# Performance work log

Measured on AMD Instinct MI355X. Metric: run time of the kernel, lower is better.

The kernel has to match this reference:

```python
import jax, jax.numpy as jnp
import numpy as np

B, D, F, K, S = 256, 1024, 4096, 8, 8  # batch, d_model, d_ffn, basis_count, cluster_size


def setup_inputs() -> dict:
    key = jax.random.key(0)
    ks = jax.random.split(key, 7)
    return {
        "x": jax.random.normal(ks[0], (B, D, 1, 1), dtype=jnp.float32),
        "gate_w": jax.random.normal(ks[1], (K, F, D), dtype=jnp.float32) * (D ** -0.5),
        "up_w": jax.random.normal(ks[2], (K, F, D), dtype=jnp.float32) * (D ** -0.5),
        "down_w": jax.random.normal(ks[3], (K, D, F), dtype=jnp.float32) * (F ** -0.5),
        "gate_coeff": jax.random.normal(ks[4], (S, K), dtype=jnp.float32) * (K ** -0.5),
        "up_coeff": jax.random.normal(ks[5], (S, K), dtype=jnp.float32) * (K ** -0.5),
        "down_coeff": jax.random.normal(ks[6], (S, K), dtype=jnp.float32) * (K ** -0.5),
    }


def reference(x, gate_w, up_w, down_w, gate_coeff, up_coeff, down_coeff):
    # x: [B, D, 1, 1] -> token vectors [B, D]  (1x1 convs == matmuls; conv biases are zero)
    b = x.shape[0]
    xs = x[:, :, 0, 0]
    # basis banks: [B, K, F]
    gate_bank = jnp.einsum('bd,kfd->bkf', xs, gate_w)
    up_bank = jnp.einsum('bd,kfd->bkf', xs, up_w)
    # per-slot coefficient contraction over basis dim K -> [B, S, F]
    gate = jnp.einsum('bkf,sk->bsf', gate_bank, gate_coeff)
    up = jnp.einsum('bkf,sk->bsf', up_bank, up_coeff)
    hidden = jax.nn.silu(gate) * up  # [B, S, F]
    # down basis bank: [B, S, K, D]
    down_bank = jnp.einsum('bsf,kdf->bskd', hidden, down_w)
    out = jnp.einsum('bskd,sk->bsd', down_bank, down_coeff)  # [B, S, D]
    # torch.cat over slots along channel dim -> [B, S*D, 1, 1]
    return out.reshape(b, -1, 1, 1)
```

## Files before the change

### kernel.cpp

```cpp
#include <hip/hip_runtime.h>

#define B_SZ 256
#define D_SZ 1024
#define F_SZ 4096
#define K_SZ 8
#define S_SZ 8
#define NW   (2 * K_SZ * F_SZ)
#define SD   (S_SZ * D_SZ)

typedef __attribute__((ext_vector_type(4))) float f32x4v;
typedef __attribute__((ext_vector_type(8))) short s16x8v;

#define SWZ(row, col) ((col) ^ (((row) & 7) << 3))

#define BAR() do {                                            \
    asm volatile("s_waitcnt lgkmcnt(0)" ::: "memory");        \
    __builtin_amdgcn_sched_barrier(0);                        \
    __builtin_amdgcn_s_barrier();                             \
    __builtin_amdgcn_sched_barrier(0);                        \
} while (0)

static __device__ __forceinline__ unsigned short f2bf(float f) {
    union { float f; unsigned u; } v; v.f = f;
    unsigned u = v.u;
    unsigned r = u + 0x7FFFu + ((u >> 16) & 1u);
    return (unsigned short)(r >> 16);
}
static __device__ __forceinline__ float bf2f(unsigned short h) {
    union { unsigned u; float f; } v; v.u = ((unsigned)h) << 16;
    return v.f;
}

__global__ __launch_bounds__(256) void k_cvt_x(const float* __restrict__ x,
                                               unsigned short* __restrict__ xs) {
    int g = blockIdx.x * 256 + threadIdx.x;
    float4 v = reinterpret_cast<const float4*>(x)[g];
    ushort4 h;
    h.x = f2bf(v.x); h.y = f2bf(v.y); h.z = f2bf(v.z); h.w = f2bf(v.w);
    reinterpret_cast<ushort4*>(xs)[g] = h;
}

__global__ __launch_bounds__(512)
void k_bank_gemm(const unsigned short* __restrict__ xs,
                 const float* __restrict__ gw,
                 const float* __restrict__ uw,
                 unsigned short* __restrict__ bank) {
    __shared__ unsigned short As[2][256 * 64];
    __shared__ unsigned short Bs[2][128 * 64];

    const int tid  = threadIdx.x;
    const int lane = tid & 63;
    const int wid  = tid >> 6;
    const int wm   = wid >> 1;
    const int wn   = wid & 1;
    const int n0   = blockIdx.x * 128;

    const int ar = tid >> 3;
    const int ac = (tid * 8) & 63;
    const int br = tid >> 4;
    const int bc = (tid * 4) & 63;

    f32x4v acc[4][4];
    #pragma unroll
    for (int i = 0; i < 4; i++)
        #pragma unroll
        for (int j = 0; j < 4; j++) {
            f32x4v z = {0.f, 0.f, 0.f, 0.f};
            acc[i][j] = z;
        }

    uint4  a0[4], a1[4];
    float4 b0[4], b1[4];

#define K1_LOAD_A(dst, kt) do { _Pragma("unroll")                              \
    for (int i = 0; i < 4; i++)                                                \
        dst[i] = *reinterpret_cast<const uint4*>(                              \
            xs + (size_t)(ar + i * 64) * D_SZ + (kt) * 64 + ac); } while (0)

#define K1_LOAD_B(dst, kt) do { _Pragma("unroll")                              \
    for (int i = 0; i < 4; i++) {                                              \
        int n = n0 + br + i * 32;                                              \
        const float* src = (n < K_SZ * F_SZ)                                   \
            ? (gw + (size_t)n * D_SZ)                                          \
            : (uw + (size_t)(n - K_SZ * F_SZ) * D_SZ);                         \
        dst[i] = *reinterpret_cast<const float4*>(src + (kt) * 64 + bc);       \
    } } while (0)

#define K1_WRITE_A(buf, src) do { _Pragma("unroll")                            \
    for (int i = 0; i < 4; i++) {                                              \
        int r = ar + i * 64;                                                   \
        *reinterpret_cast<uint4*>(&As[buf][(r << 6) + SWZ(r, ac)]) = src[i];   \
    } } while (0)

#define K1_WRITE_B(buf, src) do { _Pragma("unroll")                            \
    for (int i = 0; i < 4; i++) {                                              \
        int r = br + i * 32; ushort4 h;                                        \
        h.x = f2bf(src[i].x); h.y = f2bf(src[i].y);                            \
        h.z = f2bf(src[i].z); h.w = f2bf(src[i].w);                            \
        *reinterpret_cast<ushort4*>(&Bs[buf][(r << 6) + SWZ(r, bc)]) = h;      \
    } } while (0)

#define K1_COMPUTE(buf) do { _Pragma("unroll")                                 \
    for (int kk = 0; kk < 2; kk++) {                                           \
        const int kof = kk * 32 + (lane >> 4) * 8;                             \
        s16x8v af[4], bfv[4];                                                  \
        _Pragma("unroll") for (int i = 0; i < 4; i++) {                        \
            int row = wm * 64 + i * 16 + (lane & 15);                          \
            af[i] = *reinterpret_cast<const s16x8v*>(                          \
                &As[buf][(row << 6) + SWZ(row, kof)]); }                       \
        _Pragma("unroll") for (int j = 0; j < 4; j++) {                        \
            int col = wn * 64 + j * 16 + (lane & 15);                          \
            bfv[j] = *reinterpret_cast<const s16x8v*>(                         \
                &Bs[buf][(col << 6) + SWZ(col, kof)]); }                       \
        _Pragma("unroll") for (int i = 0; i < 4; i++)                          \
            _Pragma("unroll") for (int j = 0; j < 4; j++)                      \
                acc[i][j] = __builtin_amdgcn_mfma_f32_16x16x32_bf16(           \
                    af[i], bfv[j], acc[i][j], 0, 0, 0);                        \
    } } while (0)

    K1_LOAD_A(a0, 0); K1_LOAD_B(b0, 0);
    K1_LOAD_A(a1, 1); K1_LOAD_B(b1, 1);
    K1_WRITE_A(0, a0); K1_WRITE_B(0, b0);
    BAR();

    #pragma unroll 1
    for (int kt2 = 0; kt2 < 8; kt2++) {
        const int kt = kt2 * 2;
        if (kt + 2 < 16) { K1_LOAD_A(a0, kt + 2); K1_LOAD_B(b0, kt + 2); }
        K1_COMPUTE(0);
        K1_WRITE_A(1, a1); K1_WRITE_B(1, b1);
        BAR();
        if (kt + 3 < 16) { K1_LOAD_A(a1, kt + 3); K1_LOAD_B(b1, kt + 3); }
        K1_COMPUTE(1);
        if (kt + 2 < 16) {
            K1_WRITE_A(0, a0); K1_WRITE_B(0, b0);
            BAR();
        }
    }

    const int r0 = (lane >> 4) * 4;
    const int c0 = lane & 15;
    #pragma unroll
    for (int i = 0; i < 4; i++) {
        int rowb = wm * 64 + i * 16 + r0;
        #pragma unroll
        for (int j = 0; j < 4; j++) {
            int col = n0 + wn * 64 + j * 16 + c0;
            #pragma unroll
            for (int r = 0; r < 4; r++)
                bank[(size_t)(rowb + r) * NW + col] = f2bf(acc[i][j][r]);
        }
    }
#undef K1_LOAD_A
#undef K1_LOAD_B
#undef K1_WRITE_A
#undef K1_WRITE_B
#undef K1_COMPUTE
}

__global__ __launch_bounds__(256)
void k_combine_silu(const unsigned short* __restrict__ bank,
                    const float* __restrict__ gcoef,
                    const float* __restrict__ ucoef,
                    unsigned short* __restrict__ hid) {
    __shared__ float sg[64], su[64];
    int tid = threadIdx.x;
    if (tid < 64) { sg[tid] = gcoef[tid]; su[tid] = ucoef[tid]; }
    __syncthreads();

    int g  = blockIdx.x * 256 + tid;
    int fq = g & (F_SZ / 4 - 1);
    int b  = g >> 10;
    size_t base = (size_t)b * NW + fq * 4;

    float gv[8][4], uv[8][4];
    #pragma unroll
    for (int k = 0; k < 8; k++) {
        ushort4 tg = *reinterpret_cast<const ushort4*>(bank + base + (size_t)k * F_SZ);
        ushort4 tu = *reinterpret_cast<const ushort4*>(bank + base + (size_t)(K_SZ * F_SZ) + (size_t)k * F_SZ);
        gv[k][0] = bf2f(tg.x); gv[k][1] = bf2f(tg.y); gv[k][2] = bf2f(tg.z); gv[k][3] = bf2f(tg.w);
        uv[k][0] = bf2f(tu.x); uv[k][1] = bf2f(tu.y); uv[k][2] = bf2f(tu.z); uv[k][3] = bf2f(tu.w);
    }
    #pragma unroll
    for (int s = 0; s < 8; s++) {
        float go[4] = {0.f, 0.f, 0.f, 0.f}, uo[4] = {0.f, 0.f, 0.f, 0.f};
        #pragma unroll
        for (int k = 0; k < 8; k++) {
            float cg = sg[s * 8 + k], cu = su[s * 8 + k];
            #pragma unroll
            for (int j = 0; j < 4; j++) {
                go[j] = fmaf(cg, gv[k][j], go[j]);
                uo[j] = fmaf(cu, uv[k][j], uo[j]);
            }
        }
        ushort4 h;
        float v0 = (go[0] / (1.f + __expf(-go[0]))) * uo[0];
        float v1 = (go[1] / (1.f + __expf(-go[1]))) * uo[1];
        float v2 = (go[2] / (1.f + __expf(-go[2]))) * uo[2];
        float v3 = (go[3] / (1.f + __expf(-go[3]))) * uo[3];
        h.x = f2bf(v0); h.y = f2bf(v1); h.z = f2bf(v2); h.w = f2bf(v3);
        *reinterpret_cast<ushort4*>(hid + ((size_t)s * B_SZ + b) * F_SZ + fq * 4) = h;
    }
}

__global__ __launch_bounds__(256)
void k_wd_combine(const float* __restrict__ dw,
                  const float* __restrict__ dcoef,
                  unsigned short* __restrict__ wd) {
    __shared__ float sd[64];
    int tid = threadIdx.x;
    if (tid < 64) sd[tid] = dcoef[tid];
    __syncthreads();

    size_t g = (size_t)blockIdx.x * 256 + tid;
    int fq = (int)(g & (F_SZ / 4 - 1));
    int d  = (int)(g >> 10);

    float wv[8][4];
    #pragma unroll
    for (int k = 0; k < 8; k++) {
        float4 t = *reinterpret_cast<const float4*>(dw + ((size_t)k * D_SZ + d) * F_SZ + fq * 4);
        wv[k][0] = t.x; wv[k][1] = t.y; wv[k][2] = t.z; wv[k][3] = t.w;
    }
    #pragma unroll
    for (int s = 0; s < 8; s++) {
        float o[4] = {0.f, 0.f, 0.f, 0.f};
        #pragma unroll
        for (int k = 0; k < 8; k++) {
            float c = sd[s * 8 + k];
            #pragma unroll
            for (int j = 0; j < 4; j++) o[j] = fmaf(c, wv[k][j], o[j]);
        }
        ushort4 h;
        h.x = f2bf(o[0]); h.y = f2bf(o[1]); h.z = f2bf(o[2]); h.w = f2bf(o[3]);
        *reinterpret_cast<ushort4*>(wd + ((size_t)s * D_SZ + d) * F_SZ + fq * 4) = h;
    }
}

__global__ __launch_bounds__(256)
void k_down_gemm(const unsigned short* __restrict__ hid,
                 const unsigned short* __restrict__ wd,
                 float* __restrict__ out) {
    __shared__ unsigned short As[2][64 * 128];
    __shared__ unsigned short Bs[2][64 * 128];

    const int tid  = threadIdx.x;
    const int lane = tid & 63;
    const int wid  = tid >> 6;
    const int wm   = wid >> 1;
    const int wn   = wid & 1;
    const int nt   = blockIdx.x;
    const int bt   = blockIdx.y;
    const int s    = blockIdx.z;

    const unsigned short* Ag = hid + (size_t)s * B_SZ * F_SZ + (size_t)bt * 64 * F_SZ;
    const unsigned short* Bg = wd  + (size_t)s * D_SZ * F_SZ + (size_t)nt * 64 * F_SZ;

    const int sr = tid >> 4;
    const int sc = (tid * 8) & 127;

    f32x4v acc[2][2];
    #pragma unroll
    for (int i = 0; i < 2; i++)
        #pragma unroll
        for (int j = 0; j < 2; j++) {
            f32x4v z = {0.f, 0.f, 0.f, 0.f};
            acc[i][j] = z;
        }

    uint4 a0[4], a1[4], b0[4], b1[4];

#define K4_LOAD(dstA, dstB, kt) do { _Pragma("unroll")                         \
    for (int i = 0; i < 4; i++) {                                              \
        int r = sr + i * 16;                                                   \
        dstA[i] = *reinterpret_cast<const uint4*>(                             \
            Ag + (size_t)r * F_SZ + (kt) * 128 + sc);                          \
        dstB[i] = *reinterpret_cast<const uint4*>(                             \
            Bg + (size_t)r * F_SZ + (kt) * 128 + sc);                          \
    } } while (0)

#define K4_WRITE(buf, srcA, srcB) do { _Pragma("unroll")                       \
    for (int i = 0; i < 4; i++) {                                              \
        int r = sr + i * 16;                                                   \
        *reinterpret_cast<uint4*>(&As[buf][(r << 7) + SWZ(r, sc)]) = srcA[i];  \
        *reinterpret_cast<uint4*>(&Bs[buf][(r << 7) + SWZ(r, sc)]) = srcB[i];  \
    } } while (0)

#define K4_COMPUTE(buf) do { _Pragma("unroll")                                 \
    for (int kk = 0; kk < 4; kk++) {                                           \
        const int kof = kk * 32 + (lane >> 4) * 8;                             \
        s16x8v af[2], bfv[2];                                                  \
        _Pragma("unroll") for (int i = 0; i < 2; i++) {                        \
            int row = wm * 32 + i * 16 + (lane & 15);                          \
            af[i] = *reinterpret_cast<const s16x8v*>(                          \
                &As[buf][(row << 7) + SWZ(row, kof)]); }                       \
        _Pragma("unroll") for (int j = 0; j < 2; j++) {                        \
            int col = wn * 32 + j * 16 + (lane & 15);                          \
            bfv[j] = *reinterpret_cast<const s16x8v*>(                         \
                &Bs[buf][(col << 7) + SWZ(col, kof)]); }                       \
        _Pragma("unroll") for (int i = 0; i < 2; i++)                          \
            _Pragma("unroll") for (int j = 0; j < 2; j++)                      \
                acc[i][j] = __builtin_amdgcn_mfma_f32_16x16x32_bf16(           \
                    af[i], bfv[j], acc[i][j], 0, 0, 0);                        \
    } } while (0)

    K4_LOAD(a0, b0, 0);
    K4_LOAD(a1, b1, 1);
    K4_WRITE(0, a0, b0);
    BAR();

    #pragma unroll 1
    for (int kt2 = 0; kt2 < 16; kt2++) {
        const int kt = kt2 * 2;
        if (kt + 2 < 32) K4_LOAD(a0, b0, kt + 2);
        K4_COMPUTE(0);
        K4_WRITE(1, a1, b1);
        BAR();
        if (kt + 3 < 32) K4_LOAD(a1, b1, kt + 3);
        K4_COMPUTE(1);
        if (kt + 2 < 32) {
            K4_WRITE(0, a0, b0);
            BAR();
        }
    }

    const int r0 = (lane >> 4) * 4;
    const int c0 = lane & 15;
    #pragma unroll
    for (int i = 0; i < 2; i++) {
        #pragma unroll
        for (int j = 0; j < 2; j++) {
            #pragma unroll
            for (int r = 0; r < 4; r++) {
                int brow = bt * 64 + wm * 32 + i * 16 + r0 + r;
                int dcol = nt * 64 + wn * 32 + j * 16 + c0;
                out[(size_t)brow * SD + (size_t)s * D_SZ + dcol] = acc[i][j][r];
            }
        }
    }
#undef K4_LOAD
#undef K4_WRITE
#undef K4_COMPUTE
}

extern "C" void kernel_launch(void* const* d_in, const int* in_sizes, int n_in,
                              void* d_out, int out_size, void* d_ws, size_t ws_size,
                              hipStream_t stream) {
    (void)in_sizes; (void)n_in; (void)out_size; (void)ws_size;

    const float* x  = (const float*)d_in[0];
    const float* gw = (const float*)d_in[1];
    const float* uw = (const float*)d_in[2];
    const float* dw = (const float*)d_in[3];
    const float* gc = (const float*)d_in[4];
    const float* uc = (const float*)d_in[5];
    const float* dc = (const float*)d_in[6];
    float* out = (float*)d_out;

    char* ws = (char*)d_ws;
    unsigned short* xs   = (unsigned short*)(ws);
    unsigned short* bank = (unsigned short*)(ws + 524288);
    unsigned short* hid  = (unsigned short*)(ws + 34078720);
    unsigned short* wdp  = (unsigned short*)(ws + 50855936);

    k_cvt_x       <<<256,  256, 0, stream>>>(x, xs);
    k_bank_gemm   <<<512,  512, 0, stream>>>(xs, gw, uw, bank);
    k_combine_silu<<<1024, 256, 0, stream>>>(bank, gc, uc, hid);
    k_wd_combine  <<<4096, 256, 0, stream>>>(dw, dc, wdp);
    k_down_gemm   <<<dim3(16, 4, 8), 256, 0, stream>>>(hid, wdp, out);
}
```

Baseline: 586.6 us.

## Stage GEMM tiles via global_load_lds, shrink tiles, remap down-GEMM blocks

Both GEMM kernels now copy A (and the down-GEMM's B) straight from global memory into LDS with global_load_lds, skipping the register round trip. The bank GEMM N-tile is halved to 64, which doubles the grid. The down GEMM uses a 64-wide K step with a flat 1D grid remapped so neighbouring blocks share tiles across XCDs. The XOR swizzle is removed, which risks LDS bank conflicts on the fragment reads, and there are twice as many barrier-synchronised iterations.

```diff
diff --git a/kernel.cpp b/kernel.cpp
--- a/kernel.cpp
+++ b/kernel.cpp
@@ -11,14 +11,8 @@
 typedef __attribute__((ext_vector_type(4))) float f32x4v;
 typedef __attribute__((ext_vector_type(8))) short s16x8v;
 
-#define SWZ(row, col) ((col) ^ (((row) & 7) << 3))
-
-#define BAR() do {                                            \
-    asm volatile("s_waitcnt lgkmcnt(0)" ::: "memory");        \
-    __builtin_amdgcn_sched_barrier(0);                        \
-    __builtin_amdgcn_s_barrier();                             \
-    __builtin_amdgcn_sched_barrier(0);                        \
-} while (0)
+typedef __attribute__((address_space(1))) const unsigned int  gas_u32;
+typedef __attribute__((address_space(3))) unsigned int        las_u32;
 
 static __device__ __forceinline__ unsigned short f2bf(float f) {
     union { float f; unsigned u; } v; v.f = f;
@@ -46,95 +40,89 @@
                  const float* __restrict__ uw,
                  unsigned short* __restrict__ bank) {
     __shared__ unsigned short As[2][256 * 64];
-    __shared__ unsigned short Bs[2][128 * 64];
+    __shared__ unsigned short Bs[2][64 * 64];
 
     const int tid  = threadIdx.x;
     const int lane = tid & 63;
     const int wid  = tid >> 6;
     const int wm   = wid >> 1;
     const int wn   = wid & 1;
-    const int n0   = blockIdx.x * 128;
-
-    const int ar = tid >> 3;
-    const int ac = (tid * 8) & 63;
-    const int br = tid >> 4;
-    const int bc = (tid * 4) & 63;
-
-    f32x4v acc[4][4];
+    const int n0   = blockIdx.x * 64;
+
+    const int a_row = wid * 32 + (lane >> 3);
+    const int a_col = (lane & 7) * 8;
+    const int b_row = tid >> 4;
+    const int b_col = (tid & 15) * 4;
+
+    f32x4v acc[4][2];
     #pragma unroll
     for (int i = 0; i < 4; i++)
         #pragma unroll
-        for (int j = 0; j < 4; j++) {
+        for (int j = 0; j < 2; j++) {
             f32x4v z = {0.f, 0.f, 0.f, 0.f};
             acc[i][j] = z;
         }
 
-    uint4  a0[4], a1[4];
-    float4 b0[4], b1[4];
-
-#define K1_LOAD_A(dst, kt) do { _Pragma("unroll")                              \
-    for (int i = 0; i < 4; i++)                                                \
-        dst[i] = *reinterpret_cast<const uint4*>(                              \
-            xs + (size_t)(ar + i * 64) * D_SZ + (kt) * 64 + ac); } while (0)
-
-#define K1_LOAD_B(dst, kt) do { _Pragma("unroll")                              \
+    float4 breg[2];
+
+#define K1_STAGE_A(buf, kt) do { _Pragma("unroll")                             \
     for (int i = 0; i < 4; i++) {                                              \
-        int n = n0 + br + i * 32;                                              \
+        const unsigned short* g = xs + (size_t)(a_row + i * 8) * D_SZ          \
+                                     + (kt) * 64 + a_col;                      \
+        __builtin_amdgcn_global_load_lds(                                      \
+            (gas_u32*)g, (las_u32*)&As[buf][(wid * 4 + i) * 512], 16, 0, 0);   \
+    } } while (0)
+
+#define K1_LOAD_B(kt) do { _Pragma("unroll")                                   \
+    for (int i = 0; i < 2; i++) {                                              \
+        int n = n0 + b_row + i * 32;                                           \
         const float* src = (n < K_SZ * F_SZ)                                   \
             ? (gw + (size_t)n * D_SZ)                                          \
             : (uw + (size_t)(n - K_SZ * F_SZ) * D_SZ);                         \
-        dst[i] = *reinterpret_cast<const float4*>(src + (kt) * 64 + bc);       \
-    } } while (0)
-
-#define K1_WRITE_A(buf, src) do { _Pragma("unroll")                            \
-    for (int i = 0; i < 4; i++) {                                              \
-        int r = ar + i * 64;                                                   \
-        *reinterpret_cast<uint4*>(&As[buf][(r << 6) + SWZ(r, ac)]) = src[i];   \
-    } } while (0)
-
-#define K1_WRITE_B(buf, src) do { _Pragma("unroll")                            \
-    for (int i = 0; i < 4; i++) {                                              \
-        int r = br + i * 32; ushort4 h;                                        \
-        h.x = f2bf(src[i].x); h.y = f2bf(src[i].y);                            \
-        h.z = f2bf(src[i].z); h.w = f2bf(src[i].w);                            \
-        *reinterpret_cast<ushort4*>(&Bs[buf][(r << 6) + SWZ(r, bc)]) = h;      \
+        breg[i] = *reinterpret_cast<const float4*>(src + (kt) * 64 + b_col);   \
+    } } while (0)
+
+#define K1_WRITE_B(buf) do { _Pragma("unroll")                                 \
+    for (int i = 0; i < 2; i++) {                                              \
+        ushort4 h;                                                             \
+        h.x = f2bf(breg[i].x); h.y = f2bf(breg[i].y);                          \
+        h.z = f2bf(breg[i].z); h.w = f2bf(breg[i].w);                          \
+        *reinterpret_cast<ushort4*>(                                           \
+            &Bs[buf][(b_row + i * 32) * 64 + b_col]) = h;                      \
     } } while (0)
 
 #define K1_COMPUTE(buf) do { _Pragma("unroll")                                 \
     for (int kk = 0; kk < 2; kk++) {                                           \
         const int kof = kk * 32 + (lane >> 4) * 8;                             \
-        s16x8v af[4], bfv[4];                                                  \
+        s16x8v af[4], bfv[2];                                                  \
         _Pragma("unroll") for (int i = 0; i < 4; i++) {                        \
             int row = wm * 64 + i * 16 + (lane & 15);                          \
-            af[i] = *reinterpret_cast<const s16x8v*>(                          \
-                &As[buf][(row << 6) + SWZ(row, kof)]); }                       \
-        _Pragma("unroll") for (int j = 0; j < 4; j++) {                        \
-            int col = wn * 64 + j * 16 + (lane & 15);                          \
-            bfv[j] = *reinterpret_cast<const s16x8v*>(                         \
-                &Bs[buf][(col << 6) + SWZ(col, kof)]); }                       \
+            af[i] = *reinterpret_cast<const s16x8v*>(&As[buf][row * 64 + kof]); } \
+        _Pragma("unroll") for (int j = 0; j < 2; j++) {                        \
+            int col = wn * 32 + j * 16 + (lane & 15);                          \
+            bfv[j] = *reinterpret_cast<const s16x8v*>(&Bs[buf][col * 64 + kof]); } \
         _Pragma("unroll") for (int i = 0; i < 4; i++)                          \
-            _Pragma("unroll") for (int j = 0; j < 4; j++)                      \
+            _Pragma("unroll") for (int j = 0; j < 2; j++)                      \
                 acc[i][j] = __builtin_amdgcn_mfma_f32_16x16x32_bf16(           \
                     af[i], bfv[j], acc[i][j], 0, 0, 0);                        \
     } } while (0)
 
-    K1_LOAD_A(a0, 0); K1_LOAD_B(b0, 0);
-    K1_LOAD_A(a1, 1); K1_LOAD_B(b1, 1);
-    K1_WRITE_A(0, a0); K1_WRITE_B(0, b0);
-    BAR();
+    K1_STAGE_A(0, 0);
+    K1_LOAD_B(0);
+    K1_WRITE_B(0);
+    __syncthreads();
 
     #pragma unroll 1
-    for (int kt2 = 0; kt2 < 8; kt2++) {
-        const int kt = kt2 * 2;
-        if (kt + 2 < 16) { K1_LOAD_A(a0, kt + 2); K1_LOAD_B(b0, kt + 2); }
-        K1_COMPUTE(0);
-        K1_WRITE_A(1, a1); K1_WRITE_B(1, b1);
-        BAR();
-        if (kt + 3 < 16) { K1_LOAD_A(a1, kt + 3); K1_LOAD_B(b1, kt + 3); }
-        K1_COMPUTE(1);
-        if (kt + 2 < 16) {
-            K1_WRITE_A(0, a0); K1_WRITE_B(0, b0);
-            BAR();
+    for (int kt = 0; kt < 16; kt++) {
+        const int cur = kt & 1;
+        if (kt + 1 < 16) {
+            K1_STAGE_A(cur ^ 1, kt + 1);
+            K1_LOAD_B(kt + 1);
+        }
+        K1_COMPUTE(cur);
+        if (kt + 1 < 16) {
+            K1_WRITE_B(cur ^ 1);
+            __syncthreads();
         }
     }
 
@@ -144,16 +132,15 @@
     for (int i = 0; i < 4; i++) {
         int rowb = wm * 64 + i * 16 + r0;
         #pragma unroll
-        for (int j = 0; j < 4; j++) {
-            int col = n0 + wn * 64 + j * 16 + c0;
+        for (int j = 0; j < 2; j++) {
+            int col = n0 + wn * 32 + j * 16 + c0;
             #pragma unroll
             for (int r = 0; r < 4; r++)
                 bank[(size_t)(rowb + r) * NW + col] = f2bf(acc[i][j][r]);
         }
     }
-#undef K1_LOAD_A
+#undef K1_STAGE_A
 #undef K1_LOAD_B
-#undef K1_WRITE_A
 #undef K1_WRITE_B
 #undef K1_COMPUTE
 }
@@ -241,23 +228,26 @@
 void k_down_gemm(const unsigned short* __restrict__ hid,
                  const unsigned short* __restrict__ wd,
                  float* __restrict__ out) {
-    __shared__ unsigned short As[2][64 * 128];
-    __shared__ unsigned short Bs[2][64 * 128];
+    __shared__ unsigned short As[2][64 * 64];
+    __shared__ unsigned short Bs[2][64 * 64];
 
     const int tid  = threadIdx.x;
     const int lane = tid & 63;
     const int wid  = tid >> 6;
     const int wm   = wid >> 1;
     const int wn   = wid & 1;
-    const int nt   = blockIdx.x;
-    const int bt   = blockIdx.y;
-    const int s    = blockIdx.z;
+
+    const int orig = blockIdx.x;
+    const int wgid = (orig & 7) * 64 + (orig >> 3);
+    const int bt   = wgid & 3;
+    const int nt   = (wgid >> 2) & 15;
+    const int s    = wgid >> 6;
 
     const unsigned short* Ag = hid + (size_t)s * B_SZ * F_SZ + (size_t)bt * 64 * F_SZ;
     const unsigned short* Bg = wd  + (size_t)s * D_SZ * F_SZ + (size_t)nt * 64 * F_SZ;
 
-    const int sr = tid >> 4;
-    const int sc = (tid * 8) & 127;
+    const int s_row = wid * 16 + (lane >> 3);
+    const int s_col = (lane & 7) * 8;
 
     f32x4v acc[2][2];
     #pragma unroll
@@ -268,60 +258,42 @@
             acc[i][j] = z;
         }
 
-    uint4 a0[4], a1[4], b0[4], b1[4];
-
-#define K4_LOAD(dstA, dstB, kt) do { _Pragma("unroll")                         \
-    for (int i = 0; i < 4; i++) {                                              \
-        int r = sr + i * 16;                                                   \
-        dstA[i] = *reinterpret_cast<const uint4*>(                             \
-            Ag + (size_t)r * F_SZ + (kt) * 128 + sc);                          \
-        dstB[i] = *reinterpret_cast<const uint4*>(                             \
-            Bg + (size_t)r * F_SZ + (kt) * 128 + sc);                          \
-    } } while (0)
-
-#define K4_WRITE(buf, srcA, srcB) do { _Pragma("unroll")                       \
-    for (int i = 0; i < 4; i++) {                                              \
-        int r = sr + i * 16;                                                   \
-        *reinterpret_cast<uint4*>(&As[buf][(r << 7) + SWZ(r, sc)]) = srcA[i];  \
-        *reinterpret_cast<uint4*>(&Bs[buf][(r << 7) + SWZ(r, sc)]) = srcB[i];  \
+#define K4_STAGE(buf, kt) do { _Pragma("unroll")                               \
+    for (int i = 0; i < 2; i++) {                                              \
+        int row = s_row + i * 8;                                               \
+        const unsigned short* ga = Ag + (size_t)row * F_SZ + (kt) * 64 + s_col;\
+        const unsigned short* gb = Bg + (size_t)row * F_SZ + (kt) * 64 + s_col;\
+        __builtin_amdgcn_global_load_lds(                                      \
+            (gas_u32*)ga, (las_u32*)&As[buf][(wid * 2 + i) * 512], 16, 0, 0);  \
+        __builtin_amdgcn_global_load_lds(                                      \
+            (gas_u32*)gb, (las_u32*)&Bs[buf][(wid * 2 + i) * 512], 16, 0, 0);  \
     } } while (0)
 
 #define K4_COMPUTE(buf) do { _Pragma("unroll")                                 \
-    for (int kk = 0; kk < 4; kk++) {                                           \
+    for (int kk = 0; kk < 2; kk++) {                                           \
         const int kof = kk * 32 + (lane >> 4) * 8;                             \
         s16x8v af[2], bfv[2];                                                  \
         _Pragma("unroll") for (int i = 0; i < 2; i++) {                        \
             int row = wm * 32 + i * 16 + (lane & 15);                          \
-            af[i] = *reinterpret_cast<const s16x8v*>(                          \
-                &As[buf][(row << 7) + SWZ(row, kof)]); }                       \
+            af[i] = *reinterpret_cast<const s16x8v*>(&As[buf][row * 64 + kof]); } \
         _Pragma("unroll") for (int j = 0; j < 2; j++) {                        \
             int col = wn * 32 + j * 16 + (lane & 15);                          \
-            bfv[j] = *reinterpret_cast<const s16x8v*>(                         \
-                &Bs[buf][(col << 7) + SWZ(col, kof)]); }                       \
+            bfv[j] = *reinterpret_cast<const s16x8v*>(&Bs[buf][col * 64 + kof]); } \
         _Pragma("unroll") for (int i = 0; i < 2; i++)                          \
             _Pragma("unroll") for (int j = 0; j < 2; j++)                      \
                 acc[i][j] = __builtin_amdgcn_mfma_f32_16x16x32_bf16(           \
                     af[i], bfv[j], acc[i][j], 0, 0, 0);                        \
     } } while (0)
 
-    K4_LOAD(a0, b0, 0);
-    K4_LOAD(a1, b1, 1);
-    K4_WRITE(0, a0, b0);
-    BAR();
+    K4_STAGE(0, 0);
+    __syncthreads();
 
     #pragma unroll 1
-    for (int kt2 = 0; kt2 < 16; kt2++) {
-        const int kt = kt2 * 2;
-        if (kt + 2 < 32) K4_LOAD(a0, b0, kt + 2);
-        K4_COMPUTE(0);
-        K4_WRITE(1, a1, b1);
-        BAR();
-        if (kt + 3 < 32) K4_LOAD(a1, b1, kt + 3);
-        K4_COMPUTE(1);
-        if (kt + 2 < 32) {
-            K4_WRITE(0, a0, b0);
-            BAR();
-        }
+    for (int kt = 0; kt < 64; kt++) {
+        const int cur = kt & 1;
+        if (kt + 1 < 64) K4_STAGE(cur ^ 1, kt + 1);
+        K4_COMPUTE(cur);
+        if (kt + 1 < 64) __syncthreads();
     }
 
     const int r0 = (lane >> 4) * 4;
@@ -338,8 +310,7 @@
             }
         }
     }
-#undef K4_LOAD
-#undef K4_WRITE
+#undef K4_STAGE
 #undef K4_COMPUTE
 }
 
@@ -364,8 +335,8 @@
     unsigned short* wdp  = (unsigned short*)(ws + 50855936);
 
     k_cvt_x       <<<256,  256, 0, stream>>>(x, xs);
-    k_bank_gemm   <<<512,  512, 0, stream>>>(xs, gw, uw, bank);
+    k_bank_gemm   <<<1024, 512, 0, stream>>>(xs, gw, uw, bank);
     k_combine_silu<<<1024, 256, 0, stream>>>(bank, gc, uc, hid);
     k_wd_combine  <<<4096, 256, 0, stream>>>(dw, dc, wdp);
-    k_down_gemm   <<<dim3(16, 4, 8), 256, 0, stream>>>(hid, wdp, out);
-}
+    k_down_gemm   <<<512,  256, 0, stream>>>(hid, wdp, out);
+}
```

New measurement: 472.7 us. -19.4%, faster.
